# Kernel tuning notes

Measured on AMD Instinct MI355X. Metric: run time of the kernel, lower is better.

Reference implementation:

```python
import jax, jax.numpy as jnp
import numpy as np

B, T, C = 4, 2048, 1024
H, D = 16, 64          # n_head, head_dim; H*D == C
FFN = 4096
EPS = 1e-6


def rmsnorm(x, w):
    rms = jnp.sqrt(jnp.mean(x * x, axis=-1, keepdims=True) + EPS)
    return x / rms * w


def l2norm(x):
    n = jnp.sqrt(jnp.sum(x * x, axis=-1, keepdims=True))
    return x / jnp.maximum(n, 1e-12)


def setup_inputs() -> dict:
    key = jax.random.key(0)
    ks = jax.random.split(key, 16)
    s = 0.02
    inp = {
        'x': jax.random.normal(ks[0], (B, T, C), jnp.float32),
        'cos': jax.random.uniform(ks[1], (T, D // 2), jnp.float32),
        'sin': jax.random.uniform(ks[2], (T, D // 2), jnp.float32),
        'norm1_w': jnp.ones((C,), jnp.float32),
        'norm2_w': jnp.ones((C,), jnp.float32),
        'q_w': jax.random.normal(ks[3], (C, C), jnp.float32) * s,
        'k_w': jax.random.normal(ks[4], (C, C), jnp.float32) * s,
        'v_w': jax.random.normal(ks[5], (C, C), jnp.float32) * s,
        'beta_w': jax.random.normal(ks[6], (H, C), jnp.float32) * s,
        'beta_b': jnp.zeros((H,), jnp.float32),
        'gate_w': jax.random.normal(ks[7], (C, C), jnp.float32) * s,
        'o_w': jax.random.normal(ks[8], (C, C), jnp.float32) * s,
        'ffn_gate_w': jax.random.normal(ks[9], (FFN, C), jnp.float32) * s,
        'ffn_up_w': jax.random.normal(ks[10], (FFN, C), jnp.float32) * s,
        'ffn_down_w': jax.random.normal(ks[11], (C, FFN), jnp.float32) * s,
    }
    return inp


def gated_delta_net(xn, q_w, k_w, v_w, beta_w, beta_b, gate_w, o_w):
    # projections -> (B, T, H, D)
    q = (xn @ q_w.T).reshape(B, T, H, D)
    k = (xn @ k_w.T).reshape(B, T, H, D)
    v = (xn @ v_w.T).reshape(B, T, H, D)
    beta = jax.nn.sigmoid(xn @ beta_w.T + beta_b)   # (B, T, H)
    gate = jax.nn.sigmoid(xn @ gate_w.T)            # (B, T, C)
    q = l2norm(q)
    k = l2norm(k)

    # time-major for scan: (T, B, H, D)
    qs = jnp.moveaxis(q, 1, 0)
    ks = jnp.moveaxis(k, 1, 0)
    vs = jnp.moveaxis(v, 1, 0)
    bs = jnp.moveaxis(beta, 1, 0)                   # (T, B, H)

    def step(M, inp):
        q_t, k_t, v_t, b_t = inp
        o_t = jnp.einsum('bhdc,bhc->bhd', M, q_t)
        dv = v_t - jnp.einsum('bhdc,bhc->bhd', M, k_t)
        M = M + b_t[:, :, None, None] * jnp.einsum('bhd,bhc->bhdc', dv, k_t)
        return M, o_t

    M0 = jnp.zeros((B, H, D, D), xn.dtype)
    _, os = jax.lax.scan(step, M0, (qs, ks, vs, bs))  # os: (T, B, H, D)
    o = jnp.moveaxis(os, 0, 1).reshape(B, T, C)
    return (gate * o) @ o_w.T


def swiglu(xn, gate_w, up_w, down_w):
    return (jax.nn.silu(xn @ gate_w.T) * (xn @ up_w.T)) @ down_w.T


def reference(x, cos, sin, norm1_w, norm2_w, q_w, k_w, v_w, beta_w, beta_b,
              gate_w, o_w, ffn_gate_w, ffn_up_w, ffn_down_w):
    # layer_idx=0 -> GatedDeltaNet branch (cos/sin unused, as in torch module)
    x = x + gated_delta_net(rmsnorm(x, norm1_w), q_w, k_w, v_w,
                            beta_w, beta_b, gate_w, o_w)
    x = x + swiglu(rmsnorm(x, norm2_w), ffn_gate_w, ffn_up_w, ffn_down_w)
    return x
```

## Files before the change

### kernel.cpp

```cpp
#include <hip/hip_runtime.h>
#include <stdint.h>

typedef unsigned short u16;
typedef unsigned int   u32;
typedef unsigned long long u64;

typedef __bf16 bf16x8 __attribute__((ext_vector_type(8)));
typedef u16    u16x8  __attribute__((ext_vector_type(8)));
typedef u16    u16x4  __attribute__((ext_vector_type(4)));
typedef float  f32x4  __attribute__((ext_vector_type(4)));

#define BQ 4
#define TT 2048
#define CC 1024
#define HH 16
#define DD 64
#define FF 4096
#define BT 8192
#define NCH 32
#define LCH 64
#define LS 72

__device__ __forceinline__ float b2f(u16 v) {
  u32 u = ((u32)v) << 16;
  return __builtin_bit_cast(float, u);
}
__device__ __forceinline__ u16 f2b(float f) {
  u32 u = __builtin_bit_cast(u32, f);
  u32 r = (u + 0x7fffu + ((u >> 16) & 1u)) >> 16;
  return (u16)r;
}
__device__ __forceinline__ bf16x8 ld8(const u16* p) {
  return __builtin_bit_cast(bf16x8, *(const u16x8*)p);
}
__device__ __forceinline__ float sigmoidf_(float x) {
  return 1.0f / (1.0f + __expf(-x));
}

#define MFMA16(a, b, c) __builtin_amdgcn_mfma_f32_16x16x32_bf16(a, b, c, 0, 0, 0)

__global__ __launch_bounds__(256) void detect_k(const u16* __restrict__ xr,
                                                int* __restrict__ flag)
{
  __shared__ int cnt[4];
  const int tid = threadIdx.x;
  int c = 0;
  for (int i = tid; i < 4096; i += 256) {
    u16 u = xr[2 * i];
    int e = (u >> 7) & 0xFF;
    if (e >= 0x70 && e <= 0x86) ++c;
  }
#pragma unroll
  for (int m = 1; m < 64; m <<= 1) c += __shfl_xor(c, m, 64);
  if ((tid & 63) == 0) cnt[tid >> 6] = c;
  __syncthreads();
  if (tid == 0) *flag = (cnt[0] + cnt[1] + cnt[2] + cnt[3] >= 2048) ? 1 : 0;
}

struct Cvt { const void* src; u16* dst; u32 n; u32 pad; };
struct CvtArgs { Cvt d[13]; };

__global__ __launch_bounds__(256) void convert_k(CvtArgs a, const int* __restrict__ flag)
{
  const Cvt c = a.d[blockIdx.y];
  u64 i = ((u64)blockIdx.x * 256 + threadIdx.x) * 8;
  if (i >= c.n) return;
  if (*flag) {
    *(u16x8*)(c.dst + i) = *(const u16x8*)((const u16*)c.src + i);
  } else {
    const float* s = (const float*)c.src;
    u16x8 o;
#pragma unroll
    for (int e = 0; e < 8; ++e) o[e] = f2b(s[i + e]);
    *(u16x8*)(c.dst + i) = o;
  }
}

template <int MODE>
__global__ __launch_bounds__(256) void gemm_bt(
    const u16* __restrict__ A, const u16* __restrict__ Bw,
    void* __restrict__ Cv, const u16* __restrict__ res,
    int M, int N, int K, const int* __restrict__ flag)
{
  __shared__ __align__(16) u16 As[128 * 32];
  __shared__ __align__(16) u16 Bs[128 * 32];
  const int tid  = threadIdx.x;
  const int lane = tid & 63;
  const int wave = tid >> 6;
  const int bm = blockIdx.x, bn = blockIdx.y;
  const int rw = lane >> 2;
  const int kq = (lane & 3) * 8;
  const int lo = lane & 15;
  const int quad = lane >> 4;
  const int wm = wave & 1, wn = wave >> 1;

  const u16* Ag = A  + (u64)(bm * 128 + wave * 16 + rw) * K + kq;
  const u16* Bg = Bw + (u64)(bn * 128 + wave * 16 + rw) * K + kq;
  u16* As0 = As + wave * 16 * 32;
  u16* Bs0 = Bs + wave * 16 * 32;

  f32x4 acc[4][4] = {};

  for (int k0 = 0; k0 < K; k0 += 32) {
    u16x8 a0 = *(const u16x8*)(Ag + k0);
    u16x8 a1 = *(const u16x8*)(Ag + (u64)64 * K + k0);
    u16x8 b0 = *(const u16x8*)(Bg + k0);
    u16x8 b1 = *(const u16x8*)(Bg + (u64)64 * K + k0);
    __syncthreads();
    *(u16x8*)(As0 + lane * 8) = a0;
    *(u16x8*)(As0 + 64 * 32 + lane * 8) = a1;
    *(u16x8*)(Bs0 + lane * 8) = b0;
    *(u16x8*)(Bs0 + 64 * 32 + lane * 8) = b1;
    __syncthreads();
    bf16x8 af[4], bq[4];
#pragma unroll
    for (int i = 0; i < 4; ++i)
      af[i] = ld8(As + (wm * 64 + i * 16 + lo) * 32 + quad * 8);
#pragma unroll
    for (int j = 0; j < 4; ++j)
      bq[j] = ld8(Bs + (wn * 64 + j * 16 + lo) * 32 + quad * 8);
#pragma unroll
    for (int i = 0; i < 4; ++i)
#pragma unroll
      for (int j = 0; j < 4; ++j)
        acc[i][j] = MFMA16(af[i], bq[j], acc[i][j]);
  }

  u16* C16 = (u16*)Cv;
  float* C32 = (float*)Cv;
  const int f = (MODE == 2) ? *flag : 1;
#pragma unroll
  for (int i = 0; i < 4; ++i)
#pragma unroll
    for (int j = 0; j < 4; ++j)
#pragma unroll
      for (int r = 0; r < 4; ++r) {
        int row = bm * 128 + wm * 64 + i * 16 + quad * 4 + r;
        int col = bn * 128 + wn * 64 + j * 16 + lo;
        u64 off = (u64)row * N + col;
        float v = acc[i][j][r];
        if (MODE >= 1) v += b2f(res[off]);
        if (MODE == 2 && f == 0) C32[off] = v;
        else C16[off] = f2b(v);
      }
}

__global__ __launch_bounds__(256) void rmsnorm_k(
    const u16* __restrict__ x, const u16* __restrict__ w, u16* __restrict__ out)
{
  __shared__ float red[4];
  const int row = blockIdx.x, tid = threadIdx.x;
  const u16* xr = x + (u64)row * CC;
  u16x4 raw = *(const u16x4*)(xr + tid * 4);
  float v0 = b2f(raw[0]), v1 = b2f(raw[1]), v2 = b2f(raw[2]), v3 = b2f(raw[3]);
  float s = v0 * v0 + v1 * v1 + v2 * v2 + v3 * v3;
#pragma unroll
  for (int m = 1; m < 64; m <<= 1) s += __shfl_xor(s, m, 64);
  if ((tid & 63) == 0) red[tid >> 6] = s;
  __syncthreads();
  float tot = red[0] + red[1] + red[2] + red[3];
  float r = rsqrtf(tot * (1.0f / CC) + 1e-6f);
  const u16* wr = w + tid * 4;
  u16x4 o;
  o[0] = f2b(v0 * r * b2f(wr[0]));
  o[1] = f2b(v1 * r * b2f(wr[1]));
  o[2] = f2b(v2 * r * b2f(wr[2]));
  o[3] = f2b(v3 * r * b2f(wr[3]));
  *(u16x4*)(out + (u64)row * CC + tid * 4) = o;
}

__global__ __launch_bounds__(256) void l2norm_k(u16* __restrict__ q)
{
  const int row = blockIdx.x, tid = threadIdx.x;
  const int hh = tid >> 4, ss = tid & 15;
  u16* p = q + (u64)row * CC + hh * DD + ss * 4;
  u16x4 raw = *(const u16x4*)p;
  float v0 = b2f(raw[0]), v1 = b2f(raw[1]), v2 = b2f(raw[2]), v3 = b2f(raw[3]);
  float s = v0 * v0 + v1 * v1 + v2 * v2 + v3 * v3;
#pragma unroll
  for (int m = 1; m < 16; m <<= 1) s += __shfl_xor(s, m, 64);
  float sc = 1.0f / fmaxf(sqrtf(s), 1e-12f);
  u16x4 o;
  o[0] = f2b(v0 * sc); o[1] = f2b(v1 * sc);
  o[2] = f2b(v2 * sc); o[3] = f2b(v3 * sc);
  *(u16x4*)p = o;
}

__global__ __launch_bounds__(256) void beta_k(
    const u16* __restrict__ xn, const u16* __restrict__ bw,
    const u16* __restrict__ bb, float* __restrict__ beta)
{
  const int row = blockIdx.x, tid = threadIdx.x;
  const int hh = tid >> 4, ss = tid & 15;
  const u16* xr = xn + (u64)row * CC + ss * 64;
  const u16* wr = bw + (u64)hh * CC + ss * 64;
  float s = 0.f;
#pragma unroll
  for (int j = 0; j < 8; ++j) {
    u16x8 a = *(const u16x8*)(xr + j * 8);
    u16x8 c = *(const u16x8*)(wr + j * 8);
#pragma unroll
    for (int e = 0; e < 8; ++e) s += b2f(a[e]) * b2f(c[e]);
  }
#pragma unroll
  for (int m = 1; m < 16; m <<= 1) s += __shfl_xor(s, m, 64);
  if (ss == 0) beta[(u64)row * HH + hh] = sigmoidf_(s + b2f(bb[hh]));
}

__global__ __launch_bounds__(256) void chunk_pre(
    const u16* __restrict__ qn, const u16* __restrict__ kn,
    const u16* __restrict__ vn, const float* __restrict__ beta,
    u16* __restrict__ wneg, u16* __restrict__ u0m, u16* __restrict__ pm)
{
  __shared__ __align__(16) u16 Qc[64 * LS], Kc[64 * LS], Vc[64 * LS];
  __shared__ float Af[64 * 64];
  __shared__ float bet[64];
  const int tid = threadIdx.x;
  const int lane = tid & 63, wave = tid >> 6;
  const int lo = lane & 15, quad = lane >> 4;
  const int bc = blockIdx.x;
  const int bh = bc >> 5, c = bc & 31;
  const int b = bh >> 4, h = bh & 15;
  const u64 gbase = ((u64)(b * TT + c * LCH) * HH + h) * DD;
  const u64 cb = (u64)bc * 4096;

#pragma unroll
  for (int it = 0; it < 2; ++it) {
    int idx = tid + it * 256;
    int t = idx >> 3, seg = (idx & 7) * 8;
    u64 g = gbase + (u64)t * CC + seg;
    *(u16x8*)(Qc + t * LS + seg) = *(const u16x8*)(qn + g);
    *(u16x8*)(Kc + t * LS + seg) = *(const u16x8*)(kn + g);
    *(u16x8*)(Vc + t * LS + seg) = *(const u16x8*)(vn + g);
  }
  if (tid < 64) bet[tid] = beta[(u64)(b * TT + c * LCH + tid) * HH + h];
  __syncthreads();

  {
    const int wm = wave & 1, wn = wave >> 1;
    f32x4 aa[2][2] = {};
#pragma unroll
    for (int k0 = 0; k0 < 64; k0 += 32) {
      bf16x8 af[2], bq[2];
#pragma unroll
      for (int i = 0; i < 2; ++i) af[i] = ld8(Kc + (wm * 32 + i * 16 + lo) * LS + k0 + quad * 8);
#pragma unroll
      for (int j = 0; j < 2; ++j) bq[j] = ld8(Kc + (wn * 32 + j * 16 + lo) * LS + k0 + quad * 8);
#pragma unroll
      for (int i = 0; i < 2; ++i)
#pragma unroll
        for (int j = 0; j < 2; ++j) aa[i][j] = MFMA16(af[i], bq[j], aa[i][j]);
    }
#pragma unroll
    for (int i = 0; i < 2; ++i)
#pragma unroll
      for (int j = 0; j < 2; ++j)
#pragma unroll
        for (int r = 0; r < 4; ++r) {
          int t = wm * 32 + i * 16 + quad * 4 + r;
          int s = wn * 32 + j * 16 + lo;
          Af[t * 64 + s] = (s < t) ? bet[t] * aa[i][j][r] : 0.0f;
        }
  }
  __syncthreads();

  if (wave < 2) {
    const u16* src = (wave == 0) ? Kc : Vc;
    u16* dst = (wave == 0) ? wneg : u0m;
    const float sgn = (wave == 0) ? -1.0f : 1.0f;
    const int d = lane;
    float hist[64];
#pragma unroll
    for (int t = 0; t < 64; ++t) {
      float a = bet[t] * b2f(src[t * LS + d]);
#pragma unroll
      for (int s = 0; s < t; ++s) a -= Af[t * 64 + s] * hist[s];
      hist[t] = a;
      dst[cb + (u64)t * 64 + d] = f2b(sgn * a);
    }
  } else {
    const int w2 = wave - 2;
    f32x4 ap[2][4] = {};
#pragma unroll
    for (int k0 = 0; k0 < 64; k0 += 32) {
      bf16x8 af[2], bq[4];
#pragma unroll
      for (int i = 0; i < 2; ++i) af[i] = ld8(Qc + (w2 * 32 + i * 16 + lo) * LS + k0 + quad * 8);
#pragma unroll
      for (int j = 0; j < 4; ++j) bq[j] = ld8(Kc + (j * 16 + lo) * LS + k0 + quad * 8);
#pragma unroll
      for (int i = 0; i < 2; ++i)
#pragma unroll
        for (int j = 0; j < 4; ++j) ap[i][j] = MFMA16(af[i], bq[j], ap[i][j]);
    }
#pragma unroll
    for (int i = 0; i < 2; ++i)
#pragma unroll
      for (int j = 0; j < 4; ++j)
#pragma unroll
        for (int r = 0; r < 4; ++r) {
          int t = w2 * 32 + i * 16 + quad * 4 + r;
          int s = j * 16 + lo;
          pm[cb + (u64)t * 64 + s] = f2b((s < t) ? ap[i][j][r] : 0.0f);
        }
  }
}

__device__ __forceinline__ void gemm64_acc(
    f32x4 acc[2][2], const u16* Am, const u16* Bm,
    int wm, int wn, int lo, int quad)
{
#pragma unroll
  for (int k0 = 0; k0 < 64; k0 += 32) {
    bf16x8 af[2], bq[2];
#pragma unroll
    for (int i = 0; i < 2; ++i) af[i] = ld8(Am + (wm * 32 + i * 16 + lo) * LS + k0 + quad * 8);
#pragma unroll
    for (int j = 0; j < 2; ++j) bq[j] = ld8(Bm + (wn * 32 + j * 16 + lo) * LS + k0 + quad * 8);
#pragma unroll
    for (int i = 0; i < 2; ++i)
#pragma unroll
      for (int j = 0; j < 2; ++j) acc[i][j] = MFMA16(af[i], bq[j], acc[i][j]);
  }
}

__global__ __launch_bounds__(256) void chunk_seq(
    const u16* __restrict__ qn, const u16* __restrict__ kn,
    const u16* __restrict__ wneg, const u16* __restrict__ u0m,
    const u16* __restrict__ pm, u16* __restrict__ ob)
{
  __shared__ __align__(16) u16 Qs[64 * LS], KTs[64 * LS], Ws[64 * LS],
      Ps[64 * LS], U0s[64 * LS], UTs[64 * LS], Sb[64 * LS];
  const int tid = threadIdx.x;
  const int lane = tid & 63, wave = tid >> 6;
  const int lo = lane & 15, quad = lane >> 4;
  const int wm = wave & 1, wn = wave >> 1;
  const int bh = blockIdx.x;
  const int b = bh >> 4, h = bh & 15;
  f32x4 Sacc[2][2] = {};
  for (int i = tid; i < 64 * LS; i += 256) Sb[i] = 0;
  __syncthreads();

#pragma unroll 1
  for (int c = 0; c < NCH; ++c) {
    const u64 gbase = ((u64)(b * TT + c * LCH) * HH + h) * DD;
    const u64 cb = (u64)(bh * NCH + c) * 4096;
#pragma unroll
    for (int it = 0; it < 2; ++it) {
      int idx = tid + it * 256;
      int t = idx >> 3, seg = (idx & 7) * 8;
      u64 g = gbase + (u64)t * CC + seg;
      *(u16x8*)(Qs + t * LS + seg) = *(const u16x8*)(qn + g);
      u16x8 kv = *(const u16x8*)(kn + g);
#pragma unroll
      for (int jj = 0; jj < 8; ++jj) KTs[(seg + jj) * LS + t] = kv[jj];
      *(u16x8*)(Ws + t * LS + seg)  = *(const u16x8*)(wneg + cb + t * 64 + seg);
      *(u16x8*)(Ps + t * LS + seg)  = *(const u16x8*)(pm + cb + t * 64 + seg);
      *(u16x8*)(U0s + t * LS + seg) = *(const u16x8*)(u0m + cb + t * 64 + seg);
    }
    __syncthreads();

    f32x4 au[2][2];
#pragma unroll
    for (int i = 0; i < 2; ++i)
#pragma unroll
      for (int j = 0; j < 2; ++j)
#pragma unroll
        for (int r = 0; r < 4; ++r)
          au[i][j][r] = b2f(U0s[(wm * 32 + i * 16 + quad * 4 + r) * LS + wn * 32 + j * 16 + lo]);
    gemm64_acc(au, Ws, Sb, wm, wn, lo, quad);
#pragma unroll
    for (int i = 0; i < 2; ++i)
#pragma unroll
      for (int j = 0; j < 2; ++j)
#pragma unroll
        for (int r = 0; r < 4; ++r)
          UTs[(wn * 32 + j * 16 + lo) * LS + wm * 32 + i * 16 + quad * 4 + r] = f2b(au[i][j][r]);
    __syncthreads();

    f32x4 ao[2][2] = {};
    gemm64_acc(ao, Qs, Sb, wm, wn, lo, quad);
    gemm64_acc(ao, Ps, UTs, wm, wn, lo, quad);
#pragma unroll
    for (int i = 0; i < 2; ++i)
#pragma unroll
      for (int j = 0; j < 2; ++j)
#pragma unroll
        for (int r = 0; r < 4; ++r)
          ob[gbase + (u64)(wm * 32 + i * 16 + quad * 4 + r) * CC + wn * 32 + j * 16 + lo] =
              f2b(ao[i][j][r]);
    gemm64_acc(Sacc, UTs, KTs, wm, wn, lo, quad);
    __syncthreads();

#pragma unroll
    for (int i = 0; i < 2; ++i)
#pragma unroll
      for (int j = 0; j < 2; ++j)
#pragma unroll
        for (int r = 0; r < 4; ++r)
          Sb[(wm * 32 + i * 16 + quad * 4 + r) * LS + wn * 32 + j * 16 + lo] = f2b(Sacc[i][j][r]);
    __syncthreads();
  }
}

__global__ __launch_bounds__(256) void gate_mul_k(const u16* __restrict__ g,
                                                  u16* __restrict__ o, u64 n)
{
  u64 i = ((u64)blockIdx.x * 256 + threadIdx.x) * 8;
  if (i >= n) return;
  u16x8 gv = *(const u16x8*)(g + i);
  u16x8 ov = *(const u16x8*)(o + i);
  u16x8 r;
#pragma unroll
  for (int e = 0; e < 8; ++e)
    r[e] = f2b(sigmoidf_(b2f(gv[e])) * b2f(ov[e]));
  *(u16x8*)(o + i) = r;
}

__global__ __launch_bounds__(256) void silu_mul_k(u16* __restrict__ g,
                                                  const u16* __restrict__ u, u64 n)
{
  u64 i = ((u64)blockIdx.x * 256 + threadIdx.x) * 8;
  if (i >= n) return;
  u16x8 gv = *(const u16x8*)(g + i);
  u16x8 uv = *(const u16x8*)(u + i);
  u16x8 r;
#pragma unroll
  for (int e = 0; e < 8; ++e) {
    float gg = b2f(gv[e]);
    r[e] = f2b(gg * sigmoidf_(gg) * b2f(uv[e]));
  }
  *(u16x8*)(g + i) = r;
}

extern "C" void kernel_launch(void* const* d_in, const int* in_sizes, int n_in,
                              void* d_out, int out_size, void* d_ws, size_t ws_size,
                              hipStream_t stream)
{
  (void)in_sizes; (void)n_in; (void)out_size; (void)ws_size;
  char* ws = (char*)d_ws;
  const u64 SZ = (u64)BT * CC * 2;
  const u64 MB = 1ull << 20;

  u16* xn1  = (u16*)(ws + 0 * SZ);
  u16* qb   = (u16*)(ws + 1 * SZ);
  u16* kb   = (u16*)(ws + 2 * SZ);
  u16* vb   = (u16*)(ws + 3 * SZ);
  u16* grw  = (u16*)(ws + 4 * SZ);
  u16* wneg = (u16*)(ws + 5 * SZ);
  u16* u0m  = (u16*)(ws + 6 * SZ);
  u16* pmm  = (u16*)(ws + 7 * SZ);
  u16* obf  = (u16*)(ws + 8 * SZ);
  u16* x2   = (u16*)(ws + 9 * SZ);
  float* beta = (float*)(ws + 10 * SZ);
  int*  flag  = (int*)(ws + 10 * SZ + 768 * 1024);
  char* CV = ws + 10 * SZ + MB;
  u16* xc   = (u16*)(CV + 0 * MB);
  u16* qwc  = (u16*)(CV + 16 * MB);
  u16* kwc  = (u16*)(CV + 18 * MB);
  u16* vwc  = (u16*)(CV + 20 * MB);
  u16* gwc  = (u16*)(CV + 22 * MB);
  u16* owc  = (u16*)(CV + 24 * MB);
  u16* fgwc = (u16*)(CV + 26 * MB);
  u16* fuwc = (u16*)(CV + 34 * MB);
  u16* fdwc = (u16*)(CV + 42 * MB);
  u16* bwc  = (u16*)(CV + 50 * MB);
  u16* n1c  = (u16*)(CV + 50 * MB + 64 * 1024);
  u16* n2c  = (u16*)(CV + 50 * MB + 80 * 1024);
  u16* bbc  = (u16*)(CV + 50 * MB + 96 * 1024);
  u16* ffg  = (u16*)(ws + 0 * SZ);
  u16* ffu  = (u16*)(ws + 4 * SZ);
  u16* xn2  = obf;

  dim3 blk(256);
  dim3 g1(BT / 128, CC / 128);
  dim3 g2(BT / 128, FF / 128);
  u64 ne = (u64)BT * CC;
  u64 nf = (u64)BT * FF;

  detect_k<<<1, blk, 0, stream>>>((const u16*)d_in[0], flag);

  CvtArgs ca;
  ca.d[0]  = { d_in[0],  xc,   (u32)(BT * CC), 0 };
  ca.d[1]  = { d_in[5],  qwc,  (u32)(CC * CC), 0 };
  ca.d[2]  = { d_in[6],  kwc,  (u32)(CC * CC), 0 };
  ca.d[3]  = { d_in[7],  vwc,  (u32)(CC * CC), 0 };
  ca.d[4]  = { d_in[10], gwc,  (u32)(CC * CC), 0 };
  ca.d[5]  = { d_in[11], owc,  (u32)(CC * CC), 0 };
  ca.d[6]  = { d_in[12], fgwc, (u32)(FF * CC), 0 };
  ca.d[7]  = { d_in[13], fuwc, (u32)(FF * CC), 0 };
  ca.d[8]  = { d_in[14], fdwc, (u32)(CC * FF), 0 };
  ca.d[9]  = { d_in[8],  bwc,  (u32)(HH * CC), 0 };
  ca.d[10] = { d_in[3],  n1c,  (u32)CC, 0 };
  ca.d[11] = { d_in[4],  n2c,  (u32)CC, 0 };
  ca.d[12] = { d_in[9],  bbc,  (u32)HH, 0 };
  convert_k<<<dim3(4096, 13), blk, 0, stream>>>(ca, flag);

  rmsnorm_k<<<BT, blk, 0, stream>>>(xc, n1c, xn1);
  gemm_bt<0><<<g1, blk, 0, stream>>>(xn1, qwc, qb, nullptr, BT, CC, CC, nullptr);
  gemm_bt<0><<<g1, blk, 0, stream>>>(xn1, kwc, kb, nullptr, BT, CC, CC, nullptr);
  gemm_bt<0><<<g1, blk, 0, stream>>>(xn1, vwc, vb, nullptr, BT, CC, CC, nullptr);
  gemm_bt<0><<<g1, blk, 0, stream>>>(xn1, gwc, grw, nullptr, BT, CC, CC, nullptr);
  beta_k<<<BT, blk, 0, stream>>>(xn1, bwc, bbc, beta);
  l2norm_k<<<BT, blk, 0, stream>>>(qb);
  l2norm_k<<<BT, blk, 0, stream>>>(kb);
  chunk_pre<<<BQ * HH * NCH, blk, 0, stream>>>(qb, kb, vb, beta, wneg, u0m, pmm);
  chunk_seq<<<BQ * HH, blk, 0, stream>>>(qb, kb, wneg, u0m, pmm, obf);
  gate_mul_k<<<(unsigned)(ne / 8 / 256), blk, 0, stream>>>(grw, obf, ne);
  gemm_bt<1><<<g1, blk, 0, stream>>>(obf, owc, x2, xc, BT, CC, CC, nullptr);
  rmsnorm_k<<<BT, blk, 0, stream>>>(x2, n2c, xn2);
  gemm_bt<0><<<g2, blk, 0, stream>>>(xn2, fgwc, ffg, nullptr, BT, FF, CC, nullptr);
  gemm_bt<0><<<g2, blk, 0, stream>>>(xn2, fuwc, ffu, nullptr, BT, FF, CC, nullptr);
  silu_mul_k<<<(unsigned)(nf / 8 / 256), blk, 0, stream>>>(ffg, ffu, nf);
  gemm_bt<2><<<g1, blk, 0, stream>>>(ffg, fdwc, d_out, x2, BT, CC, FF, flag);
}
```

Baseline: 841.3 us.

## Split recurrent scan across value quarters, fuse SwiGLU into GEMM, use direct LDS loads

Several changes land together. The bf16/fp32 detect kernel is removed and fp32 inputs are assumed, so x is read directly as fp32 by rmsnorm and by the residual add, with no conversion pass for x. The GEMM stages tiles through global_load_lds instead of register round-trips. The SiLU-multiply is fused into the up-projection GEMM epilogue, dropping one elementwise pass over the 8192x4096 buffer. The chunked delta-rule scan is split four ways across value-column quarters, so 256 blocks run instead of 64, each wave doing a single 16x16 tile. The tradeoff is that the Q/K/W/P chunk loads are repeated by four blocks, and the in-place read/write of ffg in the fused epilogue relies on each element being read and written by the same thread.

```diff
diff --git a/kernel.cpp b/kernel.cpp
--- a/kernel.cpp
+++ b/kernel.cpp
@@ -39,48 +39,33 @@
 
 #define MFMA16(a, b, c) __builtin_amdgcn_mfma_f32_16x16x32_bf16(a, b, c, 0, 0, 0)
 
-__global__ __launch_bounds__(256) void detect_k(const u16* __restrict__ xr,
-                                                int* __restrict__ flag)
-{
-  __shared__ int cnt[4];
-  const int tid = threadIdx.x;
-  int c = 0;
-  for (int i = tid; i < 4096; i += 256) {
-    u16 u = xr[2 * i];
-    int e = (u >> 7) & 0xFF;
-    if (e >= 0x70 && e <= 0x86) ++c;
-  }
-#pragma unroll
-  for (int m = 1; m < 64; m <<= 1) c += __shfl_xor(c, m, 64);
-  if ((tid & 63) == 0) cnt[tid >> 6] = c;
-  __syncthreads();
-  if (tid == 0) *flag = (cnt[0] + cnt[1] + cnt[2] + cnt[3] >= 2048) ? 1 : 0;
-}
-
-struct Cvt { const void* src; u16* dst; u32 n; u32 pad; };
-struct CvtArgs { Cvt d[13]; };
-
-__global__ __launch_bounds__(256) void convert_k(CvtArgs a, const int* __restrict__ flag)
+__device__ __forceinline__ void stage16(const u16* g, u16* lds_base) {
+  __builtin_amdgcn_global_load_lds(
+      (const __attribute__((address_space(1))) u32*)(uintptr_t)g,
+      (__attribute__((address_space(3))) u32*)lds_base, 16, 0, 0);
+}
+
+struct Cvt { const float* src; u16* dst; u32 n; u32 pad; };
+struct CvtArgs { Cvt d[12]; };
+
+__global__ __launch_bounds__(256) void convert_k(CvtArgs a)
 {
   const Cvt c = a.d[blockIdx.y];
   u64 i = ((u64)blockIdx.x * 256 + threadIdx.x) * 8;
   if (i >= c.n) return;
-  if (*flag) {
-    *(u16x8*)(c.dst + i) = *(const u16x8*)((const u16*)c.src + i);
-  } else {
-    const float* s = (const float*)c.src;
-    u16x8 o;
-#pragma unroll
-    for (int e = 0; e < 8; ++e) o[e] = f2b(s[i + e]);
-    *(u16x8*)(c.dst + i) = o;
-  }
+  f32x4 v0 = *(const f32x4*)(c.src + i);
+  f32x4 v1 = *(const f32x4*)(c.src + i + 4);
+  u16x8 o;
+#pragma unroll
+  for (int e = 0; e < 4; ++e) { o[e] = f2b(v0[e]); o[e + 4] = f2b(v1[e]); }
+  *(u16x8*)(c.dst + i) = o;
 }
 
 template <int MODE>
 __global__ __launch_bounds__(256) void gemm_bt(
     const u16* __restrict__ A, const u16* __restrict__ Bw,
-    void* __restrict__ Cv, const u16* __restrict__ res,
-    int M, int N, int K, const int* __restrict__ flag)
+    void* __restrict__ Cv, const void* __restrict__ res,
+    int M, int N, int K)
 {
   __shared__ __align__(16) u16 As[128 * 32];
   __shared__ __align__(16) u16 Bs[128 * 32];
@@ -102,15 +87,10 @@
   f32x4 acc[4][4] = {};
 
   for (int k0 = 0; k0 < K; k0 += 32) {
-    u16x8 a0 = *(const u16x8*)(Ag + k0);
-    u16x8 a1 = *(const u16x8*)(Ag + (u64)64 * K + k0);
-    u16x8 b0 = *(const u16x8*)(Bg + k0);
-    u16x8 b1 = *(const u16x8*)(Bg + (u64)64 * K + k0);
-    __syncthreads();
-    *(u16x8*)(As0 + lane * 8) = a0;
-    *(u16x8*)(As0 + 64 * 32 + lane * 8) = a1;
-    *(u16x8*)(Bs0 + lane * 8) = b0;
-    *(u16x8*)(Bs0 + 64 * 32 + lane * 8) = b1;
+    stage16(Ag + k0, As0);
+    stage16(Ag + (u64)64 * K + k0, As0 + 64 * 32);
+    stage16(Bg + k0, Bs0);
+    stage16(Bg + (u64)64 * K + k0, Bs0 + 64 * 32);
     __syncthreads();
     bf16x8 af[4], bq[4];
 #pragma unroll
@@ -124,11 +104,13 @@
 #pragma unroll
       for (int j = 0; j < 4; ++j)
         acc[i][j] = MFMA16(af[i], bq[j], acc[i][j]);
+    __syncthreads();
   }
 
   u16* C16 = (u16*)Cv;
   float* C32 = (float*)Cv;
-  const int f = (MODE == 2) ? *flag : 1;
+  const float* R32 = (const float*)res;
+  const u16* R16 = (const u16*)res;
 #pragma unroll
   for (int i = 0; i < 4; ++i)
 #pragma unroll
@@ -139,20 +121,29 @@
         int col = bn * 128 + wn * 64 + j * 16 + lo;
         u64 off = (u64)row * N + col;
         float v = acc[i][j][r];
-        if (MODE >= 1) v += b2f(res[off]);
-        if (MODE == 2 && f == 0) C32[off] = v;
-        else C16[off] = f2b(v);
+        if (MODE == 1) { v += R32[off]; C16[off] = f2b(v); }
+        else if (MODE == 2) { v += b2f(R16[off]); C32[off] = v; }
+        else if (MODE == 3) {
+          float g = b2f(R16[off]);
+          C16[off] = f2b(g * sigmoidf_(g) * v);
+        } else C16[off] = f2b(v);
       }
 }
 
+template <int IN32>
 __global__ __launch_bounds__(256) void rmsnorm_k(
-    const u16* __restrict__ x, const u16* __restrict__ w, u16* __restrict__ out)
+    const void* __restrict__ xv, const u16* __restrict__ w, u16* __restrict__ out)
 {
   __shared__ float red[4];
   const int row = blockIdx.x, tid = threadIdx.x;
-  const u16* xr = x + (u64)row * CC;
-  u16x4 raw = *(const u16x4*)(xr + tid * 4);
-  float v0 = b2f(raw[0]), v1 = b2f(raw[1]), v2 = b2f(raw[2]), v3 = b2f(raw[3]);
+  float v0, v1, v2, v3;
+  if (IN32) {
+    f32x4 raw = *(const f32x4*)((const float*)xv + (u64)row * CC + tid * 4);
+    v0 = raw[0]; v1 = raw[1]; v2 = raw[2]; v3 = raw[3];
+  } else {
+    u16x4 raw = *(const u16x4*)((const u16*)xv + (u64)row * CC + tid * 4);
+    v0 = b2f(raw[0]); v1 = b2f(raw[1]); v2 = b2f(raw[2]); v3 = b2f(raw[3]);
+  }
   float s = v0 * v0 + v1 * v1 + v2 * v2 + v3 * v3;
 #pragma unroll
   for (int m = 1; m < 64; m <<= 1) s += __shfl_xor(s, m, 64);
@@ -306,39 +297,23 @@
   }
 }
 
-__device__ __forceinline__ void gemm64_acc(
-    f32x4 acc[2][2], const u16* Am, const u16* Bm,
-    int wm, int wn, int lo, int quad)
-{
-#pragma unroll
-  for (int k0 = 0; k0 < 64; k0 += 32) {
-    bf16x8 af[2], bq[2];
-#pragma unroll
-    for (int i = 0; i < 2; ++i) af[i] = ld8(Am + (wm * 32 + i * 16 + lo) * LS + k0 + quad * 8);
-#pragma unroll
-    for (int j = 0; j < 2; ++j) bq[j] = ld8(Bm + (wn * 32 + j * 16 + lo) * LS + k0 + quad * 8);
-#pragma unroll
-    for (int i = 0; i < 2; ++i)
-#pragma unroll
-      for (int j = 0; j < 2; ++j) acc[i][j] = MFMA16(af[i], bq[j], acc[i][j]);
-  }
-}
-
 __global__ __launch_bounds__(256) void chunk_seq(
     const u16* __restrict__ qn, const u16* __restrict__ kn,
     const u16* __restrict__ wneg, const u16* __restrict__ u0m,
     const u16* __restrict__ pm, u16* __restrict__ ob)
 {
-  __shared__ __align__(16) u16 Qs[64 * LS], KTs[64 * LS], Ws[64 * LS],
-      Ps[64 * LS], U0s[64 * LS], UTs[64 * LS], Sb[64 * LS];
+  __shared__ __align__(16) u16 Qs[64 * LS], KTs[64 * LS], Ws[64 * LS], Ps[64 * LS];
+  __shared__ __align__(16) u16 U0q[64 * 16];
+  __shared__ __align__(16) u16 Sq[16 * LS], UTq[16 * LS];
   const int tid = threadIdx.x;
   const int lane = tid & 63, wave = tid >> 6;
   const int lo = lane & 15, quad = lane >> 4;
-  const int wm = wave & 1, wn = wave >> 1;
-  const int bh = blockIdx.x;
+  const int blk = blockIdx.x;
+  const int bh = blk >> 2, q = blk & 3;
   const int b = bh >> 4, h = bh & 15;
-  f32x4 Sacc[2][2] = {};
-  for (int i = tid; i < 64 * LS; i += 256) Sb[i] = 0;
+  f32x4 Sacc = {};
+
+  for (int i = tid; i < 16 * LS; i += 256) Sq[i] = 0;
   __syncthreads();
 
 #pragma unroll 1
@@ -354,51 +329,58 @@
       u16x8 kv = *(const u16x8*)(kn + g);
 #pragma unroll
       for (int jj = 0; jj < 8; ++jj) KTs[(seg + jj) * LS + t] = kv[jj];
-      *(u16x8*)(Ws + t * LS + seg)  = *(const u16x8*)(wneg + cb + t * 64 + seg);
-      *(u16x8*)(Ps + t * LS + seg)  = *(const u16x8*)(pm + cb + t * 64 + seg);
-      *(u16x8*)(U0s + t * LS + seg) = *(const u16x8*)(u0m + cb + t * 64 + seg);
-    }
-    __syncthreads();
-
-    f32x4 au[2][2];
-#pragma unroll
-    for (int i = 0; i < 2; ++i)
-#pragma unroll
-      for (int j = 0; j < 2; ++j)
-#pragma unroll
-        for (int r = 0; r < 4; ++r)
-          au[i][j][r] = b2f(U0s[(wm * 32 + i * 16 + quad * 4 + r) * LS + wn * 32 + j * 16 + lo]);
-    gemm64_acc(au, Ws, Sb, wm, wn, lo, quad);
-#pragma unroll
-    for (int i = 0; i < 2; ++i)
-#pragma unroll
-      for (int j = 0; j < 2; ++j)
-#pragma unroll
-        for (int r = 0; r < 4; ++r)
-          UTs[(wn * 32 + j * 16 + lo) * LS + wm * 32 + i * 16 + quad * 4 + r] = f2b(au[i][j][r]);
-    __syncthreads();
-
-    f32x4 ao[2][2] = {};
-    gemm64_acc(ao, Qs, Sb, wm, wn, lo, quad);
-    gemm64_acc(ao, Ps, UTs, wm, wn, lo, quad);
-#pragma unroll
-    for (int i = 0; i < 2; ++i)
-#pragma unroll
-      for (int j = 0; j < 2; ++j)
-#pragma unroll
-        for (int r = 0; r < 4; ++r)
-          ob[gbase + (u64)(wm * 32 + i * 16 + quad * 4 + r) * CC + wn * 32 + j * 16 + lo] =
-              f2b(ao[i][j][r]);
-    gemm64_acc(Sacc, UTs, KTs, wm, wn, lo, quad);
-    __syncthreads();
-
-#pragma unroll
-    for (int i = 0; i < 2; ++i)
-#pragma unroll
-      for (int j = 0; j < 2; ++j)
-#pragma unroll
-        for (int r = 0; r < 4; ++r)
-          Sb[(wm * 32 + i * 16 + quad * 4 + r) * LS + wn * 32 + j * 16 + lo] = f2b(Sacc[i][j][r]);
+      *(u16x8*)(Ws + t * LS + seg) = *(const u16x8*)(wneg + cb + t * 64 + seg);
+      *(u16x8*)(Ps + t * LS + seg) = *(const u16x8*)(pm + cb + t * 64 + seg);
+    }
+    if (tid < 128) {
+      int t = tid >> 1, half = (tid & 1) * 8;
+      *(u16x8*)(U0q + t * 16 + half) =
+          *(const u16x8*)(u0m + cb + t * 64 + q * 16 + half);
+    }
+    __syncthreads();
+
+    f32x4 au;
+#pragma unroll
+    for (int r = 0; r < 4; ++r)
+      au[r] = b2f(U0q[(wave * 16 + quad * 4 + r) * 16 + lo]);
+#pragma unroll
+    for (int k0 = 0; k0 < 64; k0 += 32) {
+      bf16x8 af = ld8(Ws + (wave * 16 + lo) * LS + k0 + quad * 8);
+      bf16x8 bq = ld8(Sq + lo * LS + k0 + quad * 8);
+      au = MFMA16(af, bq, au);
+    }
+#pragma unroll
+    for (int r = 0; r < 4; ++r)
+      UTq[lo * LS + wave * 16 + quad * 4 + r] = f2b(au[r]);
+    __syncthreads();
+
+    f32x4 ao = {};
+#pragma unroll
+    for (int k0 = 0; k0 < 64; k0 += 32) {
+      bf16x8 af = ld8(Qs + (wave * 16 + lo) * LS + k0 + quad * 8);
+      bf16x8 bq = ld8(Sq + lo * LS + k0 + quad * 8);
+      ao = MFMA16(af, bq, ao);
+    }
+#pragma unroll
+    for (int k0 = 0; k0 < 64; k0 += 32) {
+      bf16x8 af = ld8(Ps + (wave * 16 + lo) * LS + k0 + quad * 8);
+      bf16x8 bq = ld8(UTq + lo * LS + k0 + quad * 8);
+      ao = MFMA16(af, bq, ao);
+    }
+#pragma unroll
+    for (int r = 0; r < 4; ++r)
+      ob[gbase + (u64)(wave * 16 + quad * 4 + r) * CC + q * 16 + lo] = f2b(ao[r]);
+
+#pragma unroll
+    for (int k0 = 0; k0 < 64; k0 += 32) {
+      bf16x8 af = ld8(UTq + lo * LS + k0 + quad * 8);
+      bf16x8 bq = ld8(KTs + (wave * 16 + lo) * LS + k0 + quad * 8);
+      Sacc = MFMA16(af, bq, Sacc);
+    }
+    __syncthreads();
+#pragma unroll
+    for (int r = 0; r < 4; ++r)
+      Sq[(quad * 4 + r) * LS + wave * 16 + lo] = f2b(Sacc[r]);
     __syncthreads();
   }
 }
@@ -417,27 +399,12 @@
   *(u16x8*)(o + i) = r;
 }
 
-__global__ __launch_bounds__(256) void silu_mul_k(u16* __restrict__ g,
-                                                  const u16* __restrict__ u, u64 n)
-{
-  u64 i = ((u64)blockIdx.x * 256 + threadIdx.x) * 8;
-  if (i >= n) return;
-  u16x8 gv = *(const u16x8*)(g + i);
-  u16x8 uv = *(const u16x8*)(u + i);
-  u16x8 r;
-#pragma unroll
-  for (int e = 0; e < 8; ++e) {
-    float gg = b2f(gv[e]);
-    r[e] = f2b(gg * sigmoidf_(gg) * b2f(uv[e]));
-  }
-  *(u16x8*)(g + i) = r;
-}
-
 extern "C" void kernel_launch(void* const* d_in, const int* in_sizes, int n_in,
                               void* d_out, int out_size, void* d_ws, size_t ws_size,
                               hipStream_t stream)
 {
   (void)in_sizes; (void)n_in; (void)out_size; (void)ws_size;
+  const float* x32 = (const float*)d_in[0];
   char* ws = (char*)d_ws;
   const u64 SZ = (u64)BT * CC * 2;
   const u64 MB = 1ull << 20;
@@ -453,21 +420,19 @@
   u16* obf  = (u16*)(ws + 8 * SZ);
   u16* x2   = (u16*)(ws + 9 * SZ);
   float* beta = (float*)(ws + 10 * SZ);
-  int*  flag  = (int*)(ws + 10 * SZ + 768 * 1024);
-  char* CV = ws + 10 * SZ + MB;
-  u16* xc   = (u16*)(CV + 0 * MB);
-  u16* qwc  = (u16*)(CV + 16 * MB);
-  u16* kwc  = (u16*)(CV + 18 * MB);
-  u16* vwc  = (u16*)(CV + 20 * MB);
-  u16* gwc  = (u16*)(CV + 22 * MB);
-  u16* owc  = (u16*)(CV + 24 * MB);
-  u16* fgwc = (u16*)(CV + 26 * MB);
-  u16* fuwc = (u16*)(CV + 34 * MB);
-  u16* fdwc = (u16*)(CV + 42 * MB);
-  u16* bwc  = (u16*)(CV + 50 * MB);
-  u16* n1c  = (u16*)(CV + 50 * MB + 64 * 1024);
-  u16* n2c  = (u16*)(CV + 50 * MB + 80 * 1024);
-  u16* bbc  = (u16*)(CV + 50 * MB + 96 * 1024);
+  char* CV  = ws + 10 * SZ + MB;
+  u16* qwc  = (u16*)(CV + 0 * MB);
+  u16* kwc  = (u16*)(CV + 2 * MB);
+  u16* vwc  = (u16*)(CV + 4 * MB);
+  u16* gwc  = (u16*)(CV + 6 * MB);
+  u16* owc  = (u16*)(CV + 8 * MB);
+  u16* fgwc = (u16*)(CV + 10 * MB);
+  u16* fuwc = (u16*)(CV + 18 * MB);
+  u16* fdwc = (u16*)(CV + 26 * MB);
+  u16* bwc  = (u16*)(CV + 34 * MB);
+  u16* n1c  = (u16*)(CV + 34 * MB + 64 * 1024);
+  u16* n2c  = (u16*)(CV + 34 * MB + 80 * 1024);
+  u16* bbc  = (u16*)(CV + 34 * MB + 96 * 1024);
   u16* ffg  = (u16*)(ws + 0 * SZ);
   u16* ffu  = (u16*)(ws + 4 * SZ);
   u16* xn2  = obf;
@@ -476,41 +441,36 @@
   dim3 g1(BT / 128, CC / 128);
   dim3 g2(BT / 128, FF / 128);
   u64 ne = (u64)BT * CC;
-  u64 nf = (u64)BT * FF;
-
-  detect_k<<<1, blk, 0, stream>>>((const u16*)d_in[0], flag);
 
   CvtArgs ca;
-  ca.d[0]  = { d_in[0],  xc,   (u32)(BT * CC), 0 };
-  ca.d[1]  = { d_in[5],  qwc,  (u32)(CC * CC), 0 };
-  ca.d[2]  = { d_in[6],  kwc,  (u32)(CC * CC), 0 };
-  ca.d[3]  = { d_in[7],  vwc,  (u32)(CC * CC), 0 };
-  ca.d[4]  = { d_in[10], gwc,  (u32)(CC * CC), 0 };
-  ca.d[5]  = { d_in[11], owc,  (u32)(CC * CC), 0 };
-  ca.d[6]  = { d_in[12], fgwc, (u32)(FF * CC), 0 };
-  ca.d[7]  = { d_in[13], fuwc, (u32)(FF * CC), 0 };
-  ca.d[8]  = { d_in[14], fdwc, (u32)(CC * FF), 0 };
-  ca.d[9]  = { d_in[8],  bwc,  (u32)(HH * CC), 0 };
-  ca.d[10] = { d_in[3],  n1c,  (u32)CC, 0 };
-  ca.d[11] = { d_in[4],  n2c,  (u32)CC, 0 };
-  ca.d[12] = { d_in[9],  bbc,  (u32)HH, 0 };
-  convert_k<<<dim3(4096, 13), blk, 0, stream>>>(ca, flag);
-
-  rmsnorm_k<<<BT, blk, 0, stream>>>(xc, n1c, xn1);
-  gemm_bt<0><<<g1, blk, 0, stream>>>(xn1, qwc, qb, nullptr, BT, CC, CC, nullptr);
-  gemm_bt<0><<<g1, blk, 0, stream>>>(xn1, kwc, kb, nullptr, BT, CC, CC, nullptr);
-  gemm_bt<0><<<g1, blk, 0, stream>>>(xn1, vwc, vb, nullptr, BT, CC, CC, nullptr);
-  gemm_bt<0><<<g1, blk, 0, stream>>>(xn1, gwc, grw, nullptr, BT, CC, CC, nullptr);
+  ca.d[0]  = { (const float*)d_in[5],  qwc,  (u32)(CC * CC), 0 };
+  ca.d[1]  = { (const float*)d_in[6],  kwc,  (u32)(CC * CC), 0 };
+  ca.d[2]  = { (const float*)d_in[7],  vwc,  (u32)(CC * CC), 0 };
+  ca.d[3]  = { (const float*)d_in[10], gwc,  (u32)(CC * CC), 0 };
+  ca.d[4]  = { (const float*)d_in[11], owc,  (u32)(CC * CC), 0 };
+  ca.d[5]  = { (const float*)d_in[12], fgwc, (u32)(FF * CC), 0 };
+  ca.d[6]  = { (const float*)d_in[13], fuwc, (u32)(FF * CC), 0 };
+  ca.d[7]  = { (const float*)d_in[14], fdwc, (u32)(CC * FF), 0 };
+  ca.d[8]  = { (const float*)d_in[8],  bwc,  (u32)(HH * CC), 0 };
+  ca.d[9]  = { (const float*)d_in[3],  n1c,  (u32)CC, 0 };
+  ca.d[10] = { (const float*)d_in[4],  n2c,  (u32)CC, 0 };
+  ca.d[11] = { (const float*)d_in[9],  bbc,  (u32)HH, 0 };
+  convert_k<<<dim3(2048, 12), blk, 0, stream>>>(ca);
+
+  rmsnorm_k<1><<<BT, blk, 0, stream>>>(x32, n1c, xn1);
+  gemm_bt<0><<<g1, blk, 0, stream>>>(xn1, qwc, qb, nullptr, BT, CC, CC);
+  gemm_bt<0><<<g1, blk, 0, stream>>>(xn1, kwc, kb, nullptr, BT, CC, CC);
+  gemm_bt<0><<<g1, blk, 0, stream>>>(xn1, vwc, vb, nullptr, BT, CC, CC);
+  gemm_bt<0><<<g1, blk, 0, stream>>>(xn1, gwc, grw, nullptr, BT, CC, CC);
   beta_k<<<BT, blk, 0, stream>>>(xn1, bwc, bbc, beta);
   l2norm_k<<<BT, blk, 0, stream>>>(qb);
   l2norm_k<<<BT, blk, 0, stream>>>(kb);
   chunk_pre<<<BQ * HH * NCH, blk, 0, stream>>>(qb, kb, vb, beta, wneg, u0m, pmm);
-  chunk_seq<<<BQ * HH, blk, 0, stream>>>(qb, kb, wneg, u0m, pmm, obf);
+  chunk_seq<<<BQ * HH * 4, blk, 0, stream>>>(qb, kb, wneg, u0m, pmm, obf);
   gate_mul_k<<<(unsigned)(ne / 8 / 256), blk, 0, stream>>>(grw, obf, ne);
-  gemm_bt<1><<<g1, blk, 0, stream>>>(obf, owc, x2, xc, BT, CC, CC, nullptr);
-  rmsnorm_k<<<BT, blk, 0, stream>>>(x2, n2c, xn2);
-  gemm_bt<0><<<g2, blk, 0, stream>>>(xn2, fgwc, ffg, nullptr, BT, FF, CC, nullptr);
-  gemm_bt<0><<<g2, blk, 0, stream>>>(xn2, fuwc, ffu, nullptr, BT, FF, CC, nullptr);
-  silu_mul_k<<<(unsigned)(nf / 8 / 256), blk, 0, stream>>>(ffg, ffu, nf);
-  gemm_bt<2><<<g1, blk, 0, stream>>>(ffg, fdwc, d_out, x2, BT, CC, FF, flag);
-}
+  gemm_bt<1><<<g1, blk, 0, stream>>>(obf, owc, x2, x32, BT, CC, CC);
+  rmsnorm_k<0><<<BT, blk, 0, stream>>>(x2, n2c, xn2);
+  gemm_bt<0><<<g2, blk, 0, stream>>>(xn2, fgwc, ffg, nullptr, BT, FF, CC);
+  gemm_bt<3><<<g2, blk, 0, stream>>>(xn2, fuwc, ffg, ffg, BT, FF, CC);
+  gemm_bt<2><<<g1, blk, 0, stream>>>(ffg, fdwc, d_out, x2, BT, CC, FF);
+}
```

Result: no change. 830.6 us (-1.3%).
